# Kernel tuning notes

Hardware: AMD Instinct MI355X
Metric: run time of the kernel (lower is better)

## Reference

```python
import jax, jax.numpy as jnp
import numpy as np

B, N, E, H, ID = 32, 256, 512, 8, 8
D = E // H  # head dim = 64


def setup_inputs() -> dict:
    key = jax.random.key(0)
    ks = jax.random.split(key, 6)
    s = lambda k, shape, fan_in: jax.random.normal(k, shape, jnp.float32) * (fan_in ** -0.5)
    return {
        "x": jax.random.normal(ks[0], (B, N, E), jnp.float32),
        "U": jax.random.normal(ks[1], (B, N, N, ID), jnp.float32),
        "w_qkv": s(ks[2], (3 * E, E), E),   # nn.MultiheadAttention in_proj_weight
        "b_qkv": jnp.zeros((3 * E,), jnp.float32),
        "w_out": s(ks[3], (E, E), E),       # out_proj.weight
        "b_out": jnp.zeros((E,), jnp.float32),
        "w_u": s(ks[4], (H, ID), ID),       # u_proj.weight
        "b_u": jnp.zeros((H,), jnp.float32),
    }


def reference(x, U, w_qkv, b_qkv, w_out, b_out, w_u, b_u):
    # fused QKV projection (torch MHA uses a single in_proj)
    qkv = x @ w_qkv.T + b_qkv                      # [B,N,3E]
    q, k, v = jnp.split(qkv, 3, axis=-1)
    split_heads = lambda t: t.reshape(B, N, H, D).transpose(0, 2, 1, 3)  # [B,H,N,D]
    q, k, v = split_heads(q), split_heads(k), split_heads(v)
    # interaction tensor -> one additive bias per head: [B,N,N,H] -> [B,H,N,N]
    bias = (U @ w_u.T + b_u).transpose(0, 3, 1, 2)
    logits = jnp.einsum('bhnd,bhmd->bhnm', q, k) * (D ** -0.5) + bias  # [B,H,N,N]
    attn = jax.nn.softmax(logits, axis=-1)
    o = jnp.einsum('bhnm,bhmd->bhnd', attn, v)     # [B,H,N,D]
    o = o.transpose(0, 2, 1, 3).reshape(B, N, E)
    return o @ w_out.T + b_out
```

## Files before the change

kernel.cpp:

```cpp
#include <hip/hip_runtime.h>
#include <stdint.h>

#define Bn 32
#define Nn 256
#define En 512
#define Hn 8
#define Dn 64

typedef __attribute__((ext_vector_type(8))) short bf16x8;
typedef __attribute__((ext_vector_type(4))) short bf16x4;
typedef __attribute__((ext_vector_type(4))) float f32x4;
typedef __attribute__((ext_vector_type(4))) _Float16 h4f;

__device__ __forceinline__ unsigned short f2bf(float f){
  union{float f; uint32_t i;} v; v.f = f;
  uint32_t i = v.i;
  return (unsigned short)((i + 0x7fffu + ((i>>16)&1u)) >> 16);
}

__device__ __forceinline__ void stage16(const unsigned short* g,
                                        unsigned short* lds_wave_base,
                                        unsigned short* lds_lane){
#if __has_builtin(__builtin_amdgcn_global_load_lds)
  __builtin_amdgcn_global_load_lds(
      (const __attribute__((address_space(1))) unsigned int*)g,
      (__attribute__((address_space(3))) unsigned int*)lds_wave_base, 16, 0, 0);
  (void)lds_lane;
#else
  *(bf16x8*)lds_lane = *(const bf16x8*)g;
  (void)lds_wave_base;
#endif
}

__global__ __launch_bounds__(256) void convert_x(
    const float* __restrict__ x, unsigned short* __restrict__ xb){
  size_t i = ((size_t)blockIdx.x * 256 + threadIdx.x) * 8;
  float4 a = *(const float4*)(x + i);
  float4 b = *(const float4*)(x + i + 4);
  bf16x8 p;
  p[0]=(short)f2bf(a.x); p[1]=(short)f2bf(a.y); p[2]=(short)f2bf(a.z); p[3]=(short)f2bf(a.w);
  p[4]=(short)f2bf(b.x); p[5]=(short)f2bf(b.y); p[6]=(short)f2bf(b.z); p[7]=(short)f2bf(b.w);
  *(bf16x8*)(xb + i) = p;
}

__global__ __launch_bounds__(256) void convert_all(
    const float* __restrict__ x, unsigned short* __restrict__ xb,
    const float* __restrict__ wq, unsigned short* __restrict__ wqb,
    const float* __restrict__ wo, unsigned short* __restrict__ wob){
  const int bx = blockIdx.x;
  const int tid = threadIdx.x;
  const float* src; unsigned short* dst; size_t i;
  if (bx < 2048)      { src = x;  dst = xb;  i = ((size_t)bx * 256 + tid) * 8; }
  else if (bx < 2432) { src = wq; dst = wqb; i = ((size_t)(bx-2048) * 256 + tid) * 8; }
  else                { src = wo; dst = wob; i = ((size_t)(bx-2432) * 256 + tid) * 8; }
  float4 a = *(const float4*)(src + i);
  float4 b = *(const float4*)(src + i + 4);
  bf16x8 p;
  p[0]=(short)f2bf(a.x); p[1]=(short)f2bf(a.y); p[2]=(short)f2bf(a.z); p[3]=(short)f2bf(a.w);
  p[4]=(short)f2bf(b.x); p[5]=(short)f2bf(b.y); p[6]=(short)f2bf(b.z); p[7]=(short)f2bf(b.w);
  *(bf16x8*)(dst + i) = p;
}

__global__ __launch_bounds__(256) void qkv_bias_gemm(
    const unsigned short* __restrict__ xb, const unsigned short* __restrict__ wqb,
    const float* __restrict__ bq,
    const float* __restrict__ U, const float* __restrict__ w_u,
    const float* __restrict__ b_u,
    unsigned short* __restrict__ q_ws, unsigned short* __restrict__ k_ws,
    unsigned short* __restrict__ v_ws, unsigned short* __restrict__ bias16){
  __shared__ unsigned short smem[32768];
  const int tid = threadIdx.x;
  const int blk = blockIdx.x;

  if (blk >= 768) {
    float* s_wu = (float*)smem;
    float* s_bu = (float*)(smem + 128);
    if (tid < 64) s_wu[tid] = w_u[tid];
    if (tid < 8)  s_bu[tid] = b_u[tid];
    __syncthreads();
    const int t  = (blk - 768) * 256 + tid;
    const int m_ = t & 255;
    const int n4 = (t >> 8) & 63;
    const int bb = t >> 14;
    const float* up = U + ((size_t)(bb*Nn + n4*4)*Nn + m_) * 8;
    float u[4][8];
    #pragma unroll
    for (int r = 0; r < 4; ++r) {
      float4 a = *(const float4*)(up + (size_t)r * (Nn*8));
      float4 c = *(const float4*)(up + (size_t)r * (Nn*8) + 4);
      u[r][0]=a.x; u[r][1]=a.y; u[r][2]=a.z; u[r][3]=a.w;
      u[r][4]=c.x; u[r][5]=c.y; u[r][6]=c.z; u[r][7]=c.w;
    }
    const int    lane_in = ((n4 & 3) * 16 + (m_ & 15)) * 4;
    const size_t tbase   = ((size_t)(n4 >> 2) * 16 + (m_ >> 4)) * 256;
    #pragma unroll
    for (int h = 0; h < 8; ++h) {
      const float bu = s_bu[h];
      float acc[4];
      #pragma unroll
      for (int r = 0; r < 4; ++r) {
        float a = bu;
        #pragma unroll
        for (int id = 0; id < 8; ++id) a += u[r][id] * s_wu[h*8 + id];
        acc[r] = a;
      }
      h4f hv;
      hv[0]=(_Float16)acc[0]; hv[1]=(_Float16)acc[1];
      hv[2]=(_Float16)acc[2]; hv[3]=(_Float16)acc[3];
      *(h4f*)(bias16 + (size_t)(bb*Hn + h) * 65536 + tbase + lane_in) = hv;
    }
    return;
  }

  const int bx = blk % 12;
  const int by = blk / 12;
  const int row0 = by * 128, n0 = bx * 128;
  const int lane = tid & 63, wv = tid >> 6;
  const int wr = wv >> 1, wc = wv & 1;
  const int lm = lane & 15, quad = lane >> 4;
  f32x4 acc[4][4] = {};

  auto stage_tile = [&](int buf, int kc){
    const int k0 = kc * 64;
    unsigned short* sa = smem + buf * 8192;
    unsigned short* sb = smem + 16384 + buf * 8192;
    #pragma unroll
    for (int i = 0; i < 4; ++i) {
      const int ci = i*256 + tid;
      const int r = ci >> 3, c = ci & 7;
      const int sc = (c ^ (r & 7)) * 8;
      stage16(xb  + (size_t)(row0 + r)*512 + k0 + sc,
              sa + (size_t)(i*256 + wv*64)*8, sa + (size_t)ci*8);
      stage16(wqb + (size_t)(n0  + r)*512 + k0 + sc,
              sb + (size_t)(i*256 + wv*64)*8, sb + (size_t)ci*8);
    }
  };

  stage_tile(0, 0);
  #pragma unroll 1
  for (int kc = 0; kc < 8; ++kc) {
    const int cur = kc & 1;
    if (kc < 7) {
      stage_tile(cur ^ 1, kc + 1);
      asm volatile("s_waitcnt vmcnt(8)" ::: "memory");
    } else {
      asm volatile("s_waitcnt vmcnt(0)" ::: "memory");
    }
    __builtin_amdgcn_s_barrier();
    __builtin_amdgcn_sched_barrier(0);
    const unsigned short* sa = smem + cur * 8192;
    const unsigned short* sb = smem + 16384 + cur * 8192;
    #pragma unroll
    for (int ks = 0; ks < 2; ++ks) {
      bf16x8 af[4], bfr[4];
      #pragma unroll
      for (int mt = 0; mt < 4; ++mt) {
        const int r = wr*64 + mt*16 + lm;
        af[mt] = *(const bf16x8*)(sa + (size_t)r*64 + (((ks*4 + quad) ^ (r & 7)) * 8));
      }
      #pragma unroll
      for (int nt = 0; nt < 4; ++nt) {
        const int r = wc*64 + nt*16 + lm;
        bfr[nt] = *(const bf16x8*)(sb + (size_t)r*64 + (((ks*4 + quad) ^ (r & 7)) * 8));
      }
      #pragma unroll
      for (int mt = 0; mt < 4; ++mt)
        #pragma unroll
        for (int nt = 0; nt < 4; ++nt)
          acc[mt][nt] = __builtin_amdgcn_mfma_f32_16x16x32_bf16(af[mt], bfr[nt], acc[mt][nt], 0, 0, 0);
    }
    __builtin_amdgcn_sched_barrier(0);
    __builtin_amdgcn_s_barrier();
  }

  const int sec = bx >> 2;
  float bias[4];
  #pragma unroll
  for (int nt = 0; nt < 4; ++nt) bias[nt] = bq[n0 + wc*64 + nt*16 + lm];
  unsigned short* tile = smem;
  if (sec < 2) {
    const float scale = (sec == 0) ? 0.125f : 1.0f;
    #pragma unroll
    for (int nt = 0; nt < 4; ++nt) {
      const int col = wc*64 + nt*16 + lm;
      #pragma unroll
      for (int mt = 0; mt < 4; ++mt)
        #pragma unroll
        for (int r = 0; r < 4; ++r) {
          const int row = wr*64 + mt*16 + quad*4 + r;
          tile[row*136 + col] = f2bf((acc[mt][nt][r] + bias[nt]) * scale);
        }
    }
  } else {
    #pragma unroll
    for (int nt = 0; nt < 4; ++nt) {
      const int col = wc*64 + nt*16 + lm;
      #pragma unroll
      for (int mt = 0; mt < 4; ++mt)
        #pragma unroll
        for (int r = 0; r < 4; ++r) {
          const int row = wr*64 + mt*16 + quad*4 + r;
          tile[col*136 + row] = f2bf(acc[mt][nt][r] + bias[nt]);
        }
    }
  }
  __syncthreads();
  if (sec < 2) {
    unsigned short* dst = (sec == 0) ? q_ws : k_ws;
    #pragma unroll
    for (int it = 0; it < 16; ++it) {
      const int rown = it*8 + (tid >> 5);
      const int col  = (tid & 31) * 4;
      bf16x4 vv = *(const bf16x4*)(tile + rown*136 + col);
      const int c = n0 + col, ch = c & 511, h = ch >> 6, d = ch & 63;
      const int grow = row0 + rown, b = grow >> 8, n = grow & 255;
      *(bf16x4*)(dst + (((size_t)b*Hn + h)*Nn + n)*Dn + d) = vv;
    }
  } else {
    const int b = row0 >> 8, nbase = row0 & 255;
    #pragma unroll
    for (int it = 0; it < 16; ++it) {
      const int c  = it*8 + (tid >> 5);
      const int n4 = (tid & 31) * 4;
      bf16x4 vv = *(const bf16x4*)(tile + c*136 + n4);
      const int ch = (n0 - 1024) + c, h = ch >> 6, d = ch & 63;
      *(bf16x4*)(v_ws + (((size_t)b*Hn + h)*Dn + d)*Nn + nbase + n4) = vv;
    }
  }
}

__global__ __launch_bounds__(256) void oproj_gemm4(
    const unsigned short* __restrict__ o_ws, const unsigned short* __restrict__ wob,
    const float* __restrict__ bo, float* __restrict__ out){
  __shared__ unsigned short smem[24576];
  const int tid = threadIdx.x;
  const int bx = blockIdx.x;
  const int by = blockIdx.y;
  const int row0 = by * 128, n0 = bx * 64;
  const int lane = tid & 63, wv = tid >> 6;
  const int wr = wv >> 1, wc = wv & 1;
  const int lm = lane & 15, quad = lane >> 4;
  f32x4 acc[4][2] = {};

  auto stage_tile = [&](int buf, int kc){
    const int k0 = kc * 64;
    unsigned short* sa = smem + buf * 8192;
    unsigned short* sb = smem + 16384 + buf * 4096;
    #pragma unroll
    for (int i = 0; i < 4; ++i) {
      const int ci = i*256 + tid;
      const int r = ci >> 3, c = ci & 7;
      const int sc = (c ^ (r & 7)) * 8;
      stage16(o_ws + (size_t)(row0 + r)*512 + k0 + sc,
              sa + (size_t)(i*256 + wv*64)*8, sa + (size_t)ci*8);
    }
    #pragma unroll
    for (int i = 0; i < 2; ++i) {
      const int ci = i*256 + tid;
      const int r = ci >> 3, c = ci & 7;
      const int sc = (c ^ (r & 7)) * 8;
      stage16(wob + (size_t)(n0 + r)*512 + k0 + sc,
              sb + (size_t)(i*256 + wv*64)*8, sb + (size_t)ci*8);
    }
  };

  stage_tile(0, 0);
  #pragma unroll 1
  for (int kc = 0; kc < 8; ++kc) {
    const int cur = kc & 1;
    if (kc < 7) {
      stage_tile(cur ^ 1, kc + 1);
      asm volatile("s_waitcnt vmcnt(6)" ::: "memory");
    } else {
      asm volatile("s_waitcnt vmcnt(0)" ::: "memory");
    }
    __builtin_amdgcn_s_barrier();
    __builtin_amdgcn_sched_barrier(0);
    const unsigned short* sa = smem + cur * 8192;
    const unsigned short* sb = smem + 16384 + cur * 4096;
    #pragma unroll
    for (int ks = 0; ks < 2; ++ks) {
      bf16x8 af[4], bfr[2];
      #pragma unroll
      for (int mt = 0; mt < 4; ++mt) {
        const int r = wr*64 + mt*16 + lm;
        af[mt] = *(const bf16x8*)(sa + (size_t)r*64 + (((ks*4 + quad) ^ (r & 7)) * 8));
      }
      #pragma unroll
      for (int nt = 0; nt < 2; ++nt) {
        const int r = wc*32 + nt*16 + lm;
        bfr[nt] = *(const bf16x8*)(sb + (size_t)r*64 + (((ks*4 + quad) ^ (r & 7)) * 8));
      }
      #pragma unroll
      for (int mt = 0; mt < 4; ++mt)
        #pragma unroll
        for (int nt = 0; nt < 2; ++nt)
          acc[mt][nt] = __builtin_amdgcn_mfma_f32_16x16x32_bf16(af[mt], bfr[nt], acc[mt][nt], 0, 0, 0);
    }
    __builtin_amdgcn_sched_barrier(0);
    __builtin_amdgcn_s_barrier();
  }
  #pragma unroll
  for (int nt = 0; nt < 2; ++nt) {
    int c = n0 + wc*32 + nt*16 + lm;
    float bias = bo[c];
    #pragma unroll
    for (int mt = 0; mt < 4; ++mt)
      #pragma unroll
      for (int r = 0; r < 4; ++r) {
        int grow = row0 + wr*64 + mt*16 + quad*4 + r;
        out[(size_t)grow*512 + c] = acc[mt][nt][r] + bias;
      }
  }
}

__global__ __launch_bounds__(256) void attn_fast(
    const unsigned short* __restrict__ bias16,
    const unsigned short* __restrict__ q_ws, const unsigned short* __restrict__ k_ws,
    const unsigned short* __restrict__ v_ws, unsigned short* __restrict__ o_ws){
  __shared__ unsigned short s_p[4][2][16][40];
  const int tid = threadIdx.x;
  const int wv = tid >> 6, lane = tid & 63;
  const int lm = lane & 15, quad = lane >> 4;
  const int bx = blockIdx.x;
  const int g  = (bx & 7) * 8 + ((bx >> 3) >> 4);
  const int qt = (bx >> 3) & 15;
  const int b = g >> 1, hp = g & 1;
  const int h = hp * 4 + wv;
  const size_t hb = (size_t)b * Hn + h;
  const int qt0 = qt * 16;
  const unsigned short* qp = q_ws + (hb*Nn + qt0 + lm) * Dn;
  const bf16x8 qa0 = *(const bf16x8*)(qp + quad*8);
  const bf16x8 qa1 = *(const bf16x8*)(qp + 32 + quad*8);
  const unsigned short* bt = bias16 + (hb*16 + qt) * 4096 + (size_t)lane*4;
  const unsigned short* kb = k_ws + (hb*Nn + lm) * Dn + quad*8;
  const unsigned short* vb = v_ws + (hb*Dn + lm) * Nn + quad*8;
  f32x4 oa[4] = {};
  float esum[4] = {0.f, 0.f, 0.f, 0.f};
  bf16x8 kf0 = *(const bf16x8*)(kb);
  bf16x8 kf1 = *(const bf16x8*)(kb + 32);
  bf16x8 kf2 = *(const bf16x8*)(kb + 16*Dn);
  bf16x8 kf3 = *(const bf16x8*)(kb + 16*Dn + 32);
  h4f hv0 = *(const h4f*)(bt);
  h4f hv1 = *(const h4f*)(bt + 256);
  #pragma unroll 2
  for (int ck = 0; ck < 8; ++ck) {
    const unsigned short* vp = vb + ck*32;
    const bf16x8 bv0 = *(const bf16x8*)(vp);
    const bf16x8 bv1 = *(const bf16x8*)(vp + 16*Nn);
    const bf16x8 bv2 = *(const bf16x8*)(vp + 32*Nn);
    const bf16x8 bv3 = *(const bf16x8*)(vp + 48*Nn);
    f32x4 la0, la1;
    #pragma unroll
    for (int r = 0; r < 4; ++r) { la0[r] = (float)hv0[r]; la1[r] = (float)hv1[r]; }
    __builtin_amdgcn_s_setprio(1);
    la0 = __builtin_amdgcn_mfma_f32_16x16x32_bf16(qa0, kf0, la0, 0, 0, 0);
    la0 = __builtin_amdgcn_mfma_f32_16x16x32_bf16(qa1, kf1, la0, 0, 0, 0);
    la1 = __builtin_amdgcn_mfma_f32_16x16x32_bf16(qa0, kf2, la1, 0, 0, 0);
    la1 = __builtin_amdgcn_mfma_f32_16x16x32_bf16(qa1, kf3, la1, 0, 0, 0);
    __builtin_amdgcn_s_setprio(0);
    if (ck < 7) {
      const unsigned short* kn = kb + (ck + 1) * 32 * Dn;
      kf0 = *(const bf16x8*)(kn);
      kf1 = *(const bf16x8*)(kn + 32);
      kf2 = *(const bf16x8*)(kn + 16*Dn);
      kf3 = *(const bf16x8*)(kn + 16*Dn + 32);
      hv0 = *(const h4f*)(bt + (ck + 1) * 512);
      hv1 = *(const h4f*)(bt + (ck + 1) * 512 + 256);
    }
    #pragma unroll
    for (int r = 0; r < 4; ++r) {
      la0[r] = __expf(la0[r]);
      la1[r] = __expf(la1[r]);
      esum[r] += la0[r] + la1[r];
    }
    const int ps = ck & 1;
    #pragma unroll
    for (int r = 0; r < 4; ++r) {
      s_p[wv][ps][quad*4+r][lm]      = f2bf(la0[r]);
      s_p[wv][ps][quad*4+r][16 + lm] = f2bf(la1[r]);
    }
    const bf16x8 ap = *(const bf16x8*)&s_p[wv][ps][lm][quad*8];
    __builtin_amdgcn_s_setprio(1);
    oa[0] = __builtin_amdgcn_mfma_f32_16x16x32_bf16(ap, bv0, oa[0], 0, 0, 0);
    oa[1] = __builtin_amdgcn_mfma_f32_16x16x32_bf16(ap, bv1, oa[1], 0, 0, 0);
    oa[2] = __builtin_amdgcn_mfma_f32_16x16x32_bf16(ap, bv2, oa[2], 0, 0, 0);
    oa[3] = __builtin_amdgcn_mfma_f32_16x16x32_bf16(ap, bv3, oa[3], 0, 0, 0);
    __builtin_amdgcn_s_setprio(0);
  }
  #pragma unroll
  for (int r = 0; r < 4; ++r) {
    float s = esum[r];
    #pragma unroll
    for (int msk = 1; msk < 16; msk <<= 1) s += __shfl_xor(s, msk);
    const float inv = 1.0f / s;
    const int n = qt0 + quad*4 + r;
    #pragma unroll
    for (int nt = 0; nt < 4; ++nt)
      o_ws[((size_t)(b*Nn + n))*En + h*64 + nt*16 + lm] = f2bf(oa[nt][r] * inv);
  }
}

__global__ __launch_bounds__(256) void qkv_gemm(
    const unsigned short* __restrict__ xb, const float* __restrict__ wq,
    const float* __restrict__ bq,
    unsigned short* __restrict__ q_ws, unsigned short* __restrict__ k_ws,
    unsigned short* __restrict__ v_ws){
  __shared__ unsigned short s_a[128][40];
  __shared__ unsigned short s_b[128][40];
  const int tid = threadIdx.x;
  const int bx = blockIdx.x;
  const int by = blockIdx.y;
  const int row0 = by * 128, n0 = bx * 128;
  const int lane = tid & 63, wv = tid >> 6;
  const int wr = wv >> 1, wc = wv & 1;
  const int lm = lane & 15, quad = lane >> 4;
  const int sr = tid >> 3, sc4 = (tid & 7) * 4;
  f32x4 acc[4][4] = {};
  for (int kc = 0; kc < 16; ++kc) {
    const int k0 = kc * 32;
    __syncthreads();
    #pragma unroll
    for (int i = 0; i < 2; ++i) {
      int g = tid * 2 + i;
      int r = g >> 2, c8 = (g & 3) * 8;
      *(bf16x8*)&s_a[r][c8] = *(const bf16x8*)(xb + (size_t)(row0 + r)*512 + k0 + c8);
    }
    #pragma unroll
    for (int i = 0; i < 4; ++i) {
      int r = sr + i * 32;
      float4 vb = *(const float4*)(wq + (size_t)(n0 + r) * 512 + k0 + sc4);
      bf16x4 pb;
      pb[0]=(short)f2bf(vb.x); pb[1]=(short)f2bf(vb.y); pb[2]=(short)f2bf(vb.z); pb[3]=(short)f2bf(vb.w);
      *(bf16x4*)&s_b[r][sc4] = pb;
    }
    __syncthreads();
    bf16x8 af[4], bfr[4];
    #pragma unroll
    for (int mt = 0; mt < 4; ++mt) af[mt]  = *(const bf16x8*)&s_a[wr*64 + mt*16 + lm][quad*8];
    #pragma unroll
    for (int nt = 0; nt < 4; ++nt) bfr[nt] = *(const bf16x8*)&s_b[wc*64 + nt*16 + lm][quad*8];
    #pragma unroll
    for (int mt = 0; mt < 4; ++mt)
      #pragma unroll
      for (int nt = 0; nt < 4; ++nt)
        acc[mt][nt] = __builtin_amdgcn_mfma_f32_16x16x32_bf16(af[mt], bfr[nt], acc[mt][nt], 0, 0, 0);
  }
  #pragma unroll
  for (int nt = 0; nt < 4; ++nt) {
    int c = n0 + wc*64 + nt*16 + lm;
    float bias = bq[c];
    int sec = c >> 9, ch = c & 511, h = ch >> 6, d = ch & 63;
    #pragma unroll
    for (int mt = 0; mt < 4; ++mt) {
      #pragma unroll
      for (int r = 0; r < 4; ++r) {
        int grow = row0 + wr*64 + mt*16 + quad*4 + r;
        int b = grow >> 8, n = grow & 255;
        float val = acc[mt][nt][r] + bias;
        if (sec == 0)      q_ws[(((size_t)b*Hn + h)*Nn + n)*Dn + d] = f2bf(val * 0.125f);
        else if (sec == 1) k_ws[(((size_t)b*Hn + h)*Nn + n)*Dn + d] = f2bf(val);
        else               v_ws[(((size_t)b*Hn + h)*Dn + d)*Nn + n] = f2bf(val);
      }
    }
  }
}

__global__ __launch_bounds__(256) void attn_kernel(
    const float* __restrict__ U, const float* __restrict__ w_u, const float* __restrict__ b_u,
    const unsigned short* __restrict__ q_ws, const unsigned short* __restrict__ k_ws,
    const unsigned short* __restrict__ v_ws, unsigned short* __restrict__ o_ws){
  __shared__ unsigned short s_p[4][2][16][40];
  __shared__ float s_wu[64];
  __shared__ float s_bu[8];
  const int tid = threadIdx.x;
  const int wv = tid >> 6, lane = tid & 63;
  const int lm = lane & 15, quad = lane >> 4;
  const int blk = blockIdx.x;
  const int b = blk >> 4, qt0 = (blk & 15) * 16;
  if (tid < 64) s_wu[tid] = w_u[tid];
  if (tid < 8)  s_bu[tid] = b_u[tid];
  __syncthreads();
  const int h0 = wv * 2, h1 = h0 + 1;
  const size_t hb0 = (size_t)b * Hn + h0, hb1 = hb0 + 1;
  float wu0[8], wu1[8];
  #pragma unroll
  for (int i = 0; i < 8; ++i) { wu0[i] = s_wu[h0*8 + i]; wu1[i] = s_wu[h1*8 + i]; }
  const float bu0 = s_bu[h0], bu1 = s_bu[h1];
  const unsigned short* q0p = q_ws + (hb0*Nn + qt0 + lm)*Dn;
  const unsigned short* q1p = q_ws + (hb1*Nn + qt0 + lm)*Dn;
  const bf16x8 qa0 = *(const bf16x8*)(q0p + quad*8);
  const bf16x8 qa1 = *(const bf16x8*)(q0p + 32 + quad*8);
  const bf16x8 qb0 = *(const bf16x8*)(q1p + quad*8);
  const bf16x8 qb1 = *(const bf16x8*)(q1p + 32 + quad*8);
  f32x4 oa[4] = {}, ob[4] = {};
  float m0[4], m1[4], l0[4], l1[4];
  #pragma unroll
  for (int r = 0; r < 4; ++r) { m0[r] = m1[r] = -3.0e38f; l0[r] = l1[r] = 0.f; }
  const float* Ub = U + ((size_t)(b*Nn + qt0)) * Nn * 8;
  #pragma unroll 1
  for (int ck = 0; ck < 8; ++ck) {
    f32x4 la0, la1, lb0, lb1;
    #pragma unroll
    for (int t = 0; t < 2; ++t) {
      const int key0 = ck*32 + t*16;
      f32x4 c0, c1;
      #pragma unroll
      for (int r = 0; r < 4; ++r) {
        const float4* up = (const float4*)(Ub + ((size_t)(quad*4+r)*Nn + key0 + lm)*8);
        float4 ua = up[0], uc = up[1];
        c0[r] = bu0 + ua.x*wu0[0] + ua.y*wu0[1] + ua.z*wu0[2] + ua.w*wu0[3]
                    + uc.x*wu0[4] + uc.y*wu0[5] + uc.z*wu0[6] + uc.w*wu0[7];
        c1[r] = bu1 + ua.x*wu1[0] + ua.y*wu1[1] + ua.z*wu1[2] + ua.w*wu1[3]
                    + uc.x*wu1[4] + uc.y*wu1[5] + uc.z*wu1[6] + uc.w*wu1[7];
      }
      const unsigned short* k0p = k_ws + (hb0*Nn + key0 + lm)*Dn;
      const unsigned short* k1p = k_ws + (hb1*Nn + key0 + lm)*Dn;
      bf16x8 kf;
      kf = *(const bf16x8*)(k0p + quad*8);
      c0 = __builtin_amdgcn_mfma_f32_16x16x32_bf16(qa0, kf, c0, 0, 0, 0);
      kf = *(const bf16x8*)(k0p + 32 + quad*8);
      c0 = __builtin_amdgcn_mfma_f32_16x16x32_bf16(qa1, kf, c0, 0, 0, 0);
      kf = *(const bf16x8*)(k1p + quad*8);
      c1 = __builtin_amdgcn_mfma_f32_16x16x32_bf16(qb0, kf, c1, 0, 0, 0);
      kf = *(const bf16x8*)(k1p + 32 + quad*8);
      c1 = __builtin_amdgcn_mfma_f32_16x16x32_bf16(qb1, kf, c1, 0, 0, 0);
      if (t == 0) { la0 = c0; lb0 = c1; } else { la1 = c0; lb1 = c1; }
    }
    #pragma unroll
    for (int r = 0; r < 4; ++r) {
      {
        float tm = fmaxf(la0[r], la1[r]);
        #pragma unroll
        for (int msk = 1; msk < 16; msk <<= 1) tm = fmaxf(tm, __shfl_xor(tm, msk));
        float mn = fmaxf(m0[r], tm);
        float al = __expf(m0[r] - mn);
        m0[r] = mn;
        float e0 = __expf(la0[r] - mn), e1 = __expf(la1[r] - mn);
        la0[r] = e0; la1[r] = e1;
        float s = e0 + e1;
        #pragma unroll
        for (int msk = 1; msk < 16; msk <<= 1) s += __shfl_xor(s, msk);
        l0[r] = l0[r] * al + s;
        #pragma unroll
        for (int nt = 0; nt < 4; ++nt) oa[nt][r] *= al;
      }
      {
        float tm = fmaxf(lb0[r], lb1[r]);
        #pragma unroll
        for (int msk = 1; msk < 16; msk <<= 1) tm = fmaxf(tm, __shfl_xor(tm, msk));
        float mn = fmaxf(m1[r], tm);
        float al = __expf(m1[r] - mn);
        m1[r] = mn;
        float e0 = __expf(lb0[r] - mn), e1 = __expf(lb1[r] - mn);
        lb0[r] = e0; lb1[r] = e1;
        float s = e0 + e1;
        #pragma unroll
        for (int msk = 1; msk < 16; msk <<= 1) s += __shfl_xor(s, msk);
        l1[r] = l1[r] * al + s;
        #pragma unroll
        for (int nt = 0; nt < 4; ++nt) ob[nt][r] *= al;
      }
    }
    #pragma unroll
    for (int r = 0; r < 4; ++r) {
      s_p[wv][0][quad*4+r][lm]      = f2bf(la0[r]);
      s_p[wv][0][quad*4+r][16 + lm] = f2bf(la1[r]);
      s_p[wv][1][quad*4+r][lm]      = f2bf(lb0[r]);
      s_p[wv][1][quad*4+r][16 + lm] = f2bf(lb1[r]);
    }
    const bf16x8 ap0 = *(const bf16x8*)&s_p[wv][0][lm][quad*8];
    const bf16x8 ap1 = *(const bf16x8*)&s_p[wv][1][lm][quad*8];
    #pragma unroll
    for (int nt = 0; nt < 4; ++nt) {
      bf16x8 bv = *(const bf16x8*)(v_ws + (hb0*Dn + nt*16 + lm)*Nn + ck*32 + quad*8);
      oa[nt] = __builtin_amdgcn_mfma_f32_16x16x32_bf16(ap0, bv, oa[nt], 0, 0, 0);
      bv = *(const bf16x8*)(v_ws + (hb1*Dn + nt*16 + lm)*Nn + ck*32 + quad*8);
      ob[nt] = __builtin_amdgcn_mfma_f32_16x16x32_bf16(ap1, bv, ob[nt], 0, 0, 0);
    }
  }
  #pragma unroll
  for (int r = 0; r < 4; ++r) {
    const float i0 = 1.0f / l0[r], i1 = 1.0f / l1[r];
    const int n = qt0 + quad*4 + r;
    #pragma unroll
    for (int nt = 0; nt < 4; ++nt) {
      o_ws[((size_t)(b*Nn + n))*En + h0*64 + nt*16 + lm] = f2bf(oa[nt][r] * i0);
      o_ws[((size_t)(b*Nn + n))*En + h1*64 + nt*16 + lm] = f2bf(ob[nt][r] * i1);
    }
  }
}

__global__ __launch_bounds__(256) void oproj_gemm(
    const unsigned short* __restrict__ o_ws, const float* __restrict__ wo,
    const float* __restrict__ bo, float* __restrict__ out){
  __shared__ unsigned short s_a[128][40];
  __shared__ unsigned short s_b[128][40];
  const int tid = threadIdx.x;
  const int bx = blockIdx.x;
  const int by = blockIdx.y;
  const int row0 = by * 128, n0 = bx * 128;
  const int lane = tid & 63, wv = tid >> 6;
  const int wr = wv >> 1, wc = wv & 1;
  const int lm = lane & 15, quad = lane >> 4;
  const int sr = tid >> 3, sc4 = (tid & 7) * 4;
  f32x4 acc[4][4] = {};
  for (int kc = 0; kc < 16; ++kc) {
    const int k0 = kc * 32;
    __syncthreads();
    #pragma unroll
    for (int i = 0; i < 2; ++i) {
      int g = tid * 2 + i;
      int r = g >> 2, c8 = (g & 3) * 8;
      *(bf16x8*)&s_a[r][c8] = *(const bf16x8*)(o_ws + (size_t)(row0 + r)*512 + k0 + c8);
    }
    #pragma unroll
    for (int i = 0; i < 4; ++i) {
      int r = sr + i * 32;
      float4 vb = *(const float4*)(wo + (size_t)(n0 + r) * 512 + k0 + sc4);
      bf16x4 pb;
      pb[0]=(short)f2bf(vb.x); pb[1]=(short)f2bf(vb.y); pb[2]=(short)f2bf(vb.z); pb[3]=(short)f2bf(vb.w);
      *(bf16x4*)&s_b[r][sc4] = pb;
    }
    __syncthreads();
    bf16x8 af[4], bfr[4];
    #pragma unroll
    for (int mt = 0; mt < 4; ++mt) af[mt]  = *(const bf16x8*)&s_a[wr*64 + mt*16 + lm][quad*8];
    #pragma unroll
    for (int nt = 0; nt < 4; ++nt) bfr[nt] = *(const bf16x8*)&s_b[wc*64 + nt*16 + lm][quad*8];
    #pragma unroll
    for (int mt = 0; mt < 4; ++mt)
      #pragma unroll
      for (int nt = 0; nt < 4; ++nt)
        acc[mt][nt] = __builtin_amdgcn_mfma_f32_16x16x32_bf16(af[mt], bfr[nt], acc[mt][nt], 0, 0, 0);
  }
  #pragma unroll
  for (int nt = 0; nt < 4; ++nt) {
    int c = n0 + wc*64 + nt*16 + lm;
    float bias = bo[c];
    #pragma unroll
    for (int mt = 0; mt < 4; ++mt)
      #pragma unroll
      for (int r = 0; r < 4; ++r) {
        int grow = row0 + wr*64 + mt*16 + quad*4 + r;
        out[(size_t)grow*512 + c] = acc[mt][nt][r] + bias;
      }
  }
}

extern "C" void kernel_launch(void* const* d_in, const int* in_sizes, int n_in,
                              void* d_out, int out_size, void* d_ws, size_t ws_size,
                              hipStream_t stream) {
  const float* x     = (const float*)d_in[0];
  const float* U     = (const float*)d_in[1];
  const float* w_qkv = (const float*)d_in[2];
  const float* b_qkv = (const float*)d_in[3];
  const float* w_out = (const float*)d_in[4];
  const float* b_out = (const float*)d_in[5];
  const float* w_u   = (const float*)d_in[6];
  const float* b_u   = (const float*)d_in[7];
  float* out = (float*)d_out;

  const size_t per = (size_t)Bn * Hn * Nn * Dn;
  unsigned short* q_ws = (unsigned short*)d_ws;
  unsigned short* k_ws = q_ws + per;
  unsigned short* v_ws = k_ws + per;
  unsigned short* o_ws = v_ws + per;
  unsigned short* bias16 = o_ws + per;
  unsigned short* wqb = bias16 + (size_t)Bn*Hn*Nn*Nn;
  unsigned short* wob = wqb + (size_t)3*En*En;

  const size_t need = (per*4 + (size_t)Bn*Hn*Nn*Nn + (size_t)3*En*En + (size_t)En*En) * 2;

  if (ws_size >= need) {
    convert_all<<<dim3(2560),  dim3(256), 0, stream>>>(x, o_ws, w_qkv, wqb, w_out, wob);
    qkv_bias_gemm<<<dim3(2816), dim3(256), 0, stream>>>(o_ws, wqb, b_qkv, U, w_u, b_u,
                                                        q_ws, k_ws, v_ws, bias16);
    attn_fast <<<dim3(1024),   dim3(256), 0, stream>>>(bias16, q_ws, k_ws, v_ws, o_ws);
    oproj_gemm4<<<dim3(8, 64), dim3(256), 0, stream>>>(o_ws, wob, b_out, out);
  } else {
    convert_x <<<dim3(2048),  dim3(256), 0, stream>>>(x, o_ws);
    qkv_gemm  <<<dim3(12, 64), dim3(256), 0, stream>>>(o_ws, w_qkv, b_qkv, q_ws, k_ws, v_ws);
    attn_kernel<<<dim3(Bn * 16), dim3(256), 0, stream>>>(U, w_u, b_u, q_ws, k_ws, v_ws, o_ws);
    oproj_gemm<<<dim3(4, 64), dim3(256), 0, stream>>>(o_ws, w_out, b_out, out);
  }
}
```

Measured before the change: 191.1 us.

## Store K and V workspaces in MFMA-fragment-friendly blocked layouts

```diff
diff --git a/kernel.cpp b/kernel.cpp
--- a/kernel.cpp
+++ b/kernel.cpp
@@ -205,26 +205,40 @@
     }
   }
   __syncthreads();
-  if (sec < 2) {
-    unsigned short* dst = (sec == 0) ? q_ws : k_ws;
+  const int b = row0 >> 8, nbase = row0 & 255;
+  if (sec == 0) {
     #pragma unroll
     for (int it = 0; it < 16; ++it) {
       const int rown = it*8 + (tid >> 5);
       const int col  = (tid & 31) * 4;
       bf16x4 vv = *(const bf16x4*)(tile + rown*136 + col);
-      const int c = n0 + col, ch = c & 511, h = ch >> 6, d = ch & 63;
-      const int grow = row0 + rown, b = grow >> 8, n = grow & 255;
-      *(bf16x4*)(dst + (((size_t)b*Hn + h)*Nn + n)*Dn + d) = vv;
+      const int ch = (n0 + col) & 511, h = ch >> 6, d = ch & 63;
+      const int n = nbase + rown;
+      *(bf16x4*)(q_ws + (((size_t)b*Hn + h)*Nn + n)*Dn + d) = vv;
+    }
+  } else if (sec == 1) {
+    const int h0k = (n0 - 512) >> 6;
+    const size_t hbk = (size_t)b*Hn + h0k;
+    #pragma unroll
+    for (int it = 0; it < 8; ++it) {
+      const int idx = it*256 + tid;
+      const int n = idx & 127;
+      const int combo = idx >> 7;
+      const int hh = combo >> 3, dg = combo & 7;
+      bf16x8 vv = *(const bf16x8*)(tile + n*136 + hh*64 + dg*8);
+      *(bf16x8*)(k_ws + (((hbk + hh)*8 + dg)*256 + nbase + n)*8) = vv;
     }
   } else {
-    const int b = row0 >> 8, nbase = row0 & 255;
-    #pragma unroll
-    for (int it = 0; it < 16; ++it) {
-      const int c  = it*8 + (tid >> 5);
-      const int n4 = (tid & 31) * 4;
-      bf16x4 vv = *(const bf16x4*)(tile + c*136 + n4);
-      const int ch = (n0 - 1024) + c, h = ch >> 6, d = ch & 63;
-      *(bf16x4*)(v_ws + (((size_t)b*Hn + h)*Dn + d)*Nn + nbase + n4) = vv;
+    const int h0v = (n0 - 1024) >> 6;
+    const size_t hbv = (size_t)b*Hn + h0v;
+    #pragma unroll
+    for (int it = 0; it < 8; ++it) {
+      const int idx = it*256 + tid;
+      const int d = idx & 63;
+      const int kgl = (idx >> 6) & 15;
+      const int hh = idx >> 10;
+      bf16x8 vv = *(const bf16x8*)(tile + (hh*64 + d)*136 + kgl*8);
+      *(bf16x8*)(v_ws + (((hbv + hh)*32 + (nbase >> 3) + kgl)*64 + d)*8) = vv;
     }
   }
 }
@@ -333,23 +347,23 @@
   const bf16x8 qa0 = *(const bf16x8*)(qp + quad*8);
   const bf16x8 qa1 = *(const bf16x8*)(qp + 32 + quad*8);
   const unsigned short* bt = bias16 + (hb*16 + qt) * 4096 + (size_t)lane*4;
-  const unsigned short* kb = k_ws + (hb*Nn + lm) * Dn + quad*8;
-  const unsigned short* vb = v_ws + (hb*Dn + lm) * Nn + quad*8;
+  const unsigned short* kb = k_ws + ((hb*8 + quad)*256 + lm) * 8;
+  const unsigned short* vb = v_ws + ((hb*32 + quad)*64 + lm) * 8;
   f32x4 oa[4] = {};
   float esum[4] = {0.f, 0.f, 0.f, 0.f};
   bf16x8 kf0 = *(const bf16x8*)(kb);
-  bf16x8 kf1 = *(const bf16x8*)(kb + 32);
-  bf16x8 kf2 = *(const bf16x8*)(kb + 16*Dn);
-  bf16x8 kf3 = *(const bf16x8*)(kb + 16*Dn + 32);
+  bf16x8 kf1 = *(const bf16x8*)(kb + 8192);
+  bf16x8 kf2 = *(const bf16x8*)(kb + 128);
+  bf16x8 kf3 = *(const bf16x8*)(kb + 8192 + 128);
   h4f hv0 = *(const h4f*)(bt);
   h4f hv1 = *(const h4f*)(bt + 256);
   #pragma unroll 2
   for (int ck = 0; ck < 8; ++ck) {
-    const unsigned short* vp = vb + ck*32;
+    const unsigned short* vp = vb + ck*2048;
     const bf16x8 bv0 = *(const bf16x8*)(vp);
-    const bf16x8 bv1 = *(const bf16x8*)(vp + 16*Nn);
-    const bf16x8 bv2 = *(const bf16x8*)(vp + 32*Nn);
-    const bf16x8 bv3 = *(const bf16x8*)(vp + 48*Nn);
+    const bf16x8 bv1 = *(const bf16x8*)(vp + 128);
+    const bf16x8 bv2 = *(const bf16x8*)(vp + 256);
+    const bf16x8 bv3 = *(const bf16x8*)(vp + 384);
     f32x4 la0, la1;
     #pragma unroll
     for (int r = 0; r < 4; ++r) { la0[r] = (float)hv0[r]; la1[r] = (float)hv1[r]; }
@@ -360,11 +374,11 @@
     la1 = __builtin_amdgcn_mfma_f32_16x16x32_bf16(qa1, kf3, la1, 0, 0, 0);
     __builtin_amdgcn_s_setprio(0);
     if (ck < 7) {
-      const unsigned short* kn = kb + (ck + 1) * 32 * Dn;
+      const unsigned short* kn = kb + (ck + 1) * 256;
       kf0 = *(const bf16x8*)(kn);
-      kf1 = *(const bf16x8*)(kn + 32);
-      kf2 = *(const bf16x8*)(kn + 16*Dn);
-      kf3 = *(const bf16x8*)(kn + 16*Dn + 32);
+      kf1 = *(const bf16x8*)(kn + 8192);
+      kf2 = *(const bf16x8*)(kn + 128);
+      kf3 = *(const bf16x8*)(kn + 8192 + 128);
       hv0 = *(const h4f*)(bt + (ck + 1) * 512);
       hv1 = *(const h4f*)(bt + (ck + 1) * 512 + 256);
     }
```

New measurement: 180.5 us. 5.5% less time.
